# Kernel optimization log

Hardware: AMD Instinct MI355X
Metric: run time of the kernel (lower is better)

The kernel has to match this reference:

```python
import jax, jax.numpy as jnp
import numpy as np

NUM_GRAPHS = 8
NEG_SLOPE = 0.2  # PyG GATConv default negative_slope


def gat_dense(x, W, att_src, att_dst, W_edge, att_edge, bias, agg, mask):
    """Dense-masked equivalent of PyG GATConv(edge_dim=1, add_self_loops=True,
    fill_value='mean'). mask[i,j]=True means edge src=i -> dst=j."""
    N = x.shape[0]
    H, C = att_src.shape
    h = (x @ W).reshape(N, H, C)                      # [N,H,C]
    a_s = jnp.einsum('nhc,hc->nh', h, att_src)        # alpha_src per node
    a_d = jnp.einsum('nhc,hc->nh', h, att_dst)        # alpha_dst per node
    eye = jnp.eye(N, dtype=bool)
    mask_od = mask & ~eye                             # remove_self_loops
    ev = jnp.where(mask_od, agg, 0.0)                 # edge_attr (scalar per edge)
    cnt = mask_od.sum(axis=0)                         # in-degree per dst
    mean_e = jnp.where(cnt > 0, ev.sum(axis=0) / jnp.maximum(cnt, 1), 0.0)
    ev = ev + jnp.eye(N, dtype=agg.dtype) * mean_e    # add self-loops, fill='mean' per dst
    full = mask_od | eye
    # lin_edge is Linear(1, H*C, bias=False): per-head edge score is
    # e_ij * sum_c W_edge[h,c]*att_edge[h,c]
    we = (W_edge.reshape(H, C) * att_edge).sum(-1)    # [H]
    logits = jax.nn.leaky_relu(a_s[:, None, :] + a_d[None, :, :] + ev[:, :, None] * we[None, None, :], NEG_SLOPE)  # [src,dst,H]
    logits = jnp.where(full[:, :, None], logits, -jnp.inf)
    alpha = jax.nn.softmax(logits, axis=0)            # segment softmax over sources per dst
    out = jnp.einsum('sdh,shc->dhc', alpha, h).reshape(N, H * C) + bias
    return out


def setup_inputs() -> dict:
    key = jax.random.key(0)
    ks = jax.random.split(key, 20)
    N, IN, HID, H, OUT = 2048, 128, 64, 4, 10
    s = 0.05
    rn = lambda k, shp, sc=s: (jax.random.normal(k, shp, dtype=jnp.float32) * sc)
    return {
        'x': jax.random.normal(ks[0], (N, IN), dtype=jnp.float32),
        'attn_tensor': jax.random.normal(ks[1], (12, N, N), dtype=jnp.float32),
        'batch_idx': jnp.sort(jax.random.randint(ks[2], (N,), 0, NUM_GRAPHS)),
        # Conv2d(12,1,1) -> 1x1 conv == weighted sum over the 12 maps
        'w_agg': rn(ks[3], (12,), 0.2),
        'b_agg': jnp.zeros((), dtype=jnp.float32),
        # GAT layer 1: in=128 -> heads=4, out=64, concat
        'W1': rn(ks[4], (IN, H * HID)),
        'att_src1': rn(ks[5], (H, HID)),
        'att_dst1': rn(ks[6], (H, HID)),
        'We1': rn(ks[7], (1, H * HID)),
        'att_e1': rn(ks[8], (H, HID)),
        'bias1': jnp.zeros((H * HID,), dtype=jnp.float32),
        # GAT layer 2: in=256 -> heads=1, out=64
        'W2': rn(ks[9], (H * HID, HID)),
        'att_src2': rn(ks[10], (1, HID)),
        'att_dst2': rn(ks[11], (1, HID)),
        'We2': rn(ks[12], (1, HID)),
        'att_e2': rn(ks[13], (1, HID)),
        'bias2': jnp.zeros((HID,), dtype=jnp.float32),
        # final Linear(hidden, out)
        'W_lin': rn(ks[14], (HID, OUT)),
        'b_lin': jnp.zeros((OUT,), dtype=jnp.float32),
    }


def reference(x, attn_tensor, batch_idx, w_agg, b_agg, W1, att_src1, att_dst1,
              We1, att_e1, bias1, W2, att_src2, att_dst2, We2, att_e2, bias2,
              W_lin, b_lin):
    # 1x1 conv over the 12 attention maps -> [N,N]
    agg = jnp.einsum('k,kij->ij', w_agg, attn_tensor) + b_agg
    mask = agg > 0.0  # threshold
    h1 = jax.nn.elu(gat_dense(x, W1, att_src1, att_dst1, We1, att_e1, bias1, agg, mask))
    h2 = jax.nn.elu(gat_dense(h1, W2, att_src2, att_dst2, We2, att_e2, bias2, agg, mask))
    # global mean pool over graphs
    ones = jnp.ones((x.shape[0],), dtype=h2.dtype)
    cnt = jax.ops.segment_sum(ones, batch_idx, num_segments=NUM_GRAPHS)
    g = jax.ops.segment_sum(h2, batch_idx, num_segments=NUM_GRAPHS) / jnp.maximum(cnt, 1.0)[:, None]
    out = g @ W_lin + b_lin
    # edge_attr = agg[mask]; returned densely (masked) to keep static shapes
    edge_attr = jnp.where(mask, agg, 0.0)
    return out, edge_attr
```

## Files before the change

kernel.cpp:

```cpp
#include <hip/hip_runtime.h>

#define N 2048
#define NG 8

__device__ __forceinline__ float lrelu(float x) { return x > 0.f ? x : 0.2f * x; }

__global__ __launch_bounds__(256) void aggh1K(const float* __restrict__ attn,
                                              const float* __restrict__ w_agg,
                                              const float* __restrict__ b_agg,
                                              const float* __restrict__ x,
                                              const float* __restrict__ W1,
                                              const float* __restrict__ att_src1,
                                              const float* __restrict__ att_dst1,
                                              const float* __restrict__ We1, const float* __restrict__ att_e1,
                                              const float* __restrict__ We2, const float* __restrict__ att_e2,
                                              float* __restrict__ edge_out,
                                              float* __restrict__ colSum, float* __restrict__ colCnt,
                                              float* __restrict__ h1, float* __restrict__ a_s1, float* __restrict__ a_d1,
                                              float* __restrict__ we) {
  __shared__ float smem[512];
  int tid = threadIdx.x;
  if (blockIdx.x < 512) {
    float* xr = smem;
    int n0 = blockIdx.x * 4;
    if (blockIdx.x == 0) {
      float v1 = We1[tid] * att_e1[tid];
#pragma unroll
      for (int off = 32; off > 0; off >>= 1) v1 += __shfl_down(v1, off);
      int lane = tid & 63, wid = tid >> 6;
      if (lane == 0) we[wid] = v1;
      float v2 = (tid < 64) ? We2[tid] * att_e2[tid] : 0.f;
#pragma unroll
      for (int off = 32; off > 0; off >>= 1) v2 += __shfl_down(v2, off);
      if (tid == 0) we[4] = v2;
    }
    for (int t = tid; t < 512; t += 256) xr[t] = x[n0 * 128 + t];
    __syncthreads();
    float acc[4] = {0.f, 0.f, 0.f, 0.f};
    for (int k = 0; k < 128; ++k) {
      float wv = W1[k * 256 + tid];
#pragma unroll
      for (int r = 0; r < 4; ++r) acc[r] += xr[r * 128 + k] * wv;
    }
    float asw = att_src1[tid], adw = att_dst1[tid];
    int lane = tid & 63, head = tid >> 6;
#pragma unroll
    for (int r = 0; r < 4; ++r) {
      h1[(size_t)(n0 + r) * 256 + tid] = acc[r];
      float ps = acc[r] * asw, pd = acc[r] * adw;
#pragma unroll
      for (int off = 32; off > 0; off >>= 1) { ps += __shfl_down(ps, off); pd += __shfl_down(pd, off); }
      if (lane == 0) { a_s1[(n0 + r) * 4 + head] = ps; a_d1[(n0 + r) * 4 + head] = pd; }
    }
  } else {
    float* wsh = smem;
    float* cs = smem + 32;
    float* cc = smem + 64;
    int bidA = blockIdx.x - 512;
    int tx = tid & 31, ty = tid >> 5;
    if (tid < 12) wsh[tid] = w_agg[tid];
    if (tid < 32) { cs[tid] = 0.f; cc[tid] = 0.f; }
    __syncthreads();
    int i0 = (bidA >> 6) * 32, j0 = (bidA & 63) * 32;
    int j = j0 + tx;
    float bb = b_agg[0];
#pragma unroll
    for (int r = 0; r < 4; ++r) {
      int i = i0 + ty + 8 * r;
      const float* p = attn + (size_t)i * N + j;
      float v = bb;
#pragma unroll
      for (int k = 0; k < 12; ++k) v += wsh[k] * p[(size_t)k * N * N];
      float e = v > 0.f ? v : 0.f;
      edge_out[(size_t)i * N + j] = e;
      if (e > 0.f && i != j) { atomicAdd(&cs[tx], e); atomicAdd(&cc[tx], 1.f); }
    }
    __syncthreads();
    if (tid < 32) {
      atomicAdd(&colSum[j0 + tid], cs[tid]);
      atomicAdd(&colCnt[j0 + tid], cc[tid]);
    }
  }
}

__global__ __launch_bounds__(256) void pv1K(const float* __restrict__ edge, const float* __restrict__ h1,
                                            const float* __restrict__ a_s1, const float* __restrict__ a_d1,
                                            const float* __restrict__ colSum, const float* __restrict__ colCnt,
                                            const float* __restrict__ we,
                                            float* __restrict__ partials, float* __restrict__ z1) {
  __shared__ float hT[16][260];
  __shared__ float pL[16][260];
  int tid = threadIdx.x;
  int d0 = blockIdx.x * 64;
  int sBeg = blockIdx.y * 128;
  float w0 = we[0], w1 = we[1], w2 = we[2], w3 = we[3];
  int ssp = tid & 15, dq = tid >> 4;
  float4 ad4[4];
  float me_[4];
#pragma unroll
  for (int q = 0; q < 4; ++q) {
    int d = d0 + dq * 4 + q;
    ad4[q] = *(const float4*)(a_d1 + d * 4);
    float c = colCnt[d];
    me_[q] = c > 0.f ? colSum[d] / c : 0.f;
  }
  float zac[4][4];
#pragma unroll
  for (int q = 0; q < 4; ++q)
#pragma unroll
    for (int h = 0; h < 4; ++h) zac[q][h] = 0.f;
  int dg = tid & 7;
  int cb = (tid >> 3) * 8;
  int hh = tid >> 6;
  float acc[8][8];
#pragma unroll
  for (int i = 0; i < 8; ++i)
#pragma unroll
    for (int j = 0; j < 8; ++j) acc[i][j] = 0.f;

  int c4 = (tid & 63) * 4;
  int rb = (tid >> 6) * 4;

#pragma unroll 1
  for (int s0 = sBeg; s0 < sBeg + 128; s0 += 16) {
#pragma unroll
    for (int p4 = 0; p4 < 4; ++p4) {
      int r = rb + p4;
      *(float4*)(&hT[r][c4]) = *(const float4*)(h1 + (size_t)(s0 + r) * 256 + c4);
    }
    {
      int s = s0 + ssp;
      float4 as4 = *(const float4*)(a_s1 + s * 4);
      float4 av4 = *(const float4*)(edge + (size_t)s * N + d0 + dq * 4);
      float ev_[4] = {av4.x, av4.y, av4.z, av4.w};
      float pq[4][4];
#pragma unroll
      for (int q = 0; q < 4; ++q) {
        int d = d0 + dq * 4 + q;
        float av = ev_[q];
        float ev; bool inc;
        if (s == d) { ev = me_[q]; inc = true; } else { ev = av; inc = av > 0.f; }
        float p0 = inc ? __expf(lrelu(as4.x + ad4[q].x + ev * w0)) : 0.f;
        float p1 = inc ? __expf(lrelu(as4.y + ad4[q].y + ev * w1)) : 0.f;
        float p2 = inc ? __expf(lrelu(as4.z + ad4[q].z + ev * w2)) : 0.f;
        float p3 = inc ? __expf(lrelu(as4.w + ad4[q].w + ev * w3)) : 0.f;
        pq[0][q] = p0; pq[1][q] = p1; pq[2][q] = p2; pq[3][q] = p3;
        zac[q][0] += p0; zac[q][1] += p1; zac[q][2] += p2; zac[q][3] += p3;
      }
#pragma unroll
      for (int h = 0; h < 4; ++h)
        *(float4*)(&pL[ssp][h * 64 + dq * 4]) = make_float4(pq[h][0], pq[h][1], pq[h][2], pq[h][3]);
    }
    __syncthreads();
#pragma unroll
    for (int ss = 0; ss < 16; ++ss) {
      float4 pA = *(const float4*)(&pL[ss][hh * 64 + dg * 8]);
      float4 pB = *(const float4*)(&pL[ss][hh * 64 + dg * 8 + 4]);
      float4 hA = *(const float4*)(&hT[ss][cb]);
      float4 hB = *(const float4*)(&hT[ss][cb + 4]);
      float pv[8] = {pA.x, pA.y, pA.z, pA.w, pB.x, pB.y, pB.z, pB.w};
      float hv[8] = {hA.x, hA.y, hA.z, hA.w, hB.x, hB.y, hB.z, hB.w};
#pragma unroll
      for (int di = 0; di < 8; ++di)
#pragma unroll
        for (int ci = 0; ci < 8; ++ci) acc[di][ci] += pv[di] * hv[ci];
    }
    __syncthreads();
  }
  float* outp = partials + (size_t)blockIdx.y * ((size_t)N * 256);
#pragma unroll
  for (int di = 0; di < 8; ++di) {
    size_t rowo = (size_t)(d0 + dg * 8 + di) * 256 + cb;
    *(float4*)(outp + rowo) = make_float4(acc[di][0], acc[di][1], acc[di][2], acc[di][3]);
    *(float4*)(outp + rowo + 4) = make_float4(acc[di][4], acc[di][5], acc[di][6], acc[di][7]);
  }
#pragma unroll
  for (int q = 0; q < 4; ++q)
#pragma unroll
    for (int h = 0; h < 4; ++h) {
      float v = zac[q][h];
      v += __shfl_down(v, 8); v += __shfl_down(v, 4);
      v += __shfl_down(v, 2); v += __shfl_down(v, 1);
      if (ssp == 0) atomicAdd(&z1[(d0 + dq * 4 + q) * 4 + h], v);
    }
}

__global__ __launch_bounds__(256) void h2K(const float* __restrict__ partials, const float* __restrict__ z1,
                                           const float* __restrict__ bias1,
                                           const float* __restrict__ W2,
                                           const float* __restrict__ att_src2, const float* __restrict__ att_dst2,
                                           float* __restrict__ hh2, float* __restrict__ a_s2, float* __restrict__ a_d2) {
  __shared__ float hr[4][256];
  int tid = threadIdx.x;
  int n0 = blockIdx.x * 4;
  for (int e = tid; e < 1024; e += 256) {
    int node = e >> 8, c = e & 255;
    size_t base = (size_t)(n0 + node) * 256 + c;
    float sAcc = 0.f;
#pragma unroll
    for (int q = 0; q < 16; ++q) sAcc += partials[(size_t)q * N * 256 + base];
    float a = sAcc / z1[(n0 + node) * 4 + (c >> 6)] + bias1[c];
    hr[node][c] = a > 0.f ? a : __expf(a) - 1.f;
  }
  __syncthreads();
  int c = tid & 63, nl = tid >> 6;
  float acc = 0.f;
  for (int k = 0; k < 256; ++k) acc += hr[nl][k] * W2[k * 64 + c];
  hh2[(size_t)(n0 + nl) * 64 + c] = acc;
  float ps = acc * att_src2[c], pd = acc * att_dst2[c];
#pragma unroll
  for (int off = 32; off > 0; off >>= 1) { ps += __shfl_down(ps, off); pd += __shfl_down(pd, off); }
  if (c == 0) { a_s2[n0 + nl] = ps; a_d2[n0 + nl] = pd; }
}

__global__ __launch_bounds__(256) void pv2K(const float* __restrict__ edge, const float* __restrict__ hh2,
                                            const float* __restrict__ a_s2, const float* __restrict__ a_d2,
                                            const float* __restrict__ colSum, const float* __restrict__ colCnt,
                                            const float* __restrict__ we,
                                            float* __restrict__ partials, float* __restrict__ z2) {
  __shared__ float hT[16][68];
  __shared__ float pL[16][132];
  int tid = threadIdx.x;
  int d0 = blockIdx.x * 128;
  int sBeg = blockIdx.y * 64;
  float wE = we[4];
  int ssp = tid & 15, dq = tid >> 4;
  float adv[8], me_[8];
#pragma unroll
  for (int q = 0; q < 8; ++q) {
    int d = d0 + dq * 8 + q;
    adv[q] = a_d2[d];
    float c = colCnt[d];
    me_[q] = c > 0.f ? colSum[d] / c : 0.f;
  }
  float zac[8];
#pragma unroll
  for (int q = 0; q < 8; ++q) zac[q] = 0.f;
  int dg = tid & 15;
  int cg = tid >> 4;
  float acc[8][4];
#pragma unroll
  for (int i = 0; i < 8; ++i)
#pragma unroll
    for (int j = 0; j < 4; ++j) acc[i][j] = 0.f;

  int stR = tid >> 4, stC = (tid & 15) * 4;

#pragma unroll 1
  for (int s0 = sBeg; s0 < sBeg + 64; s0 += 16) {
    *(float4*)(&hT[stR][stC]) = *(const float4*)(hh2 + (size_t)(s0 + stR) * 64 + stC);
    {
      int s = s0 + ssp;
      float asv = a_s2[s];
      float4 eA = *(const float4*)(edge + (size_t)s * N + d0 + dq * 8);
      float4 eB = *(const float4*)(edge + (size_t)s * N + d0 + dq * 8 + 4);
      float ev_[8] = {eA.x, eA.y, eA.z, eA.w, eB.x, eB.y, eB.z, eB.w};
      float pq[8];
#pragma unroll
      for (int q = 0; q < 8; ++q) {
        int d = d0 + dq * 8 + q;
        float av = ev_[q];
        float ev; bool inc;
        if (s == d) { ev = me_[q]; inc = true; } else { ev = av; inc = av > 0.f; }
        float p = inc ? __expf(lrelu(asv + adv[q] + ev * wE)) : 0.f;
        pq[q] = p;
        zac[q] += p;
      }
      *(float4*)(&pL[ssp][dq * 8])     = make_float4(pq[0], pq[1], pq[2], pq[3]);
      *(float4*)(&pL[ssp][dq * 8 + 4]) = make_float4(pq[4], pq[5], pq[6], pq[7]);
    }
    __syncthreads();
#pragma unroll
    for (int ss = 0; ss < 16; ++ss) {
      float4 pA = *(const float4*)(&pL[ss][dg * 8]);
      float4 pB = *(const float4*)(&pL[ss][dg * 8 + 4]);
      float4 hA = *(const float4*)(&hT[ss][cg * 4]);
      float pv[8] = {pA.x, pA.y, pA.z, pA.w, pB.x, pB.y, pB.z, pB.w};
      float hv[4] = {hA.x, hA.y, hA.z, hA.w};
#pragma unroll
      for (int di = 0; di < 8; ++di)
#pragma unroll
        for (int ci = 0; ci < 4; ++ci) acc[di][ci] += pv[di] * hv[ci];
    }
    __syncthreads();
  }
  float* outp = partials + (size_t)blockIdx.y * ((size_t)N * 64);
#pragma unroll
  for (int di = 0; di < 8; ++di) {
    size_t rowo = (size_t)(d0 + dg * 8 + di) * 64 + cg * 4;
    *(float4*)(outp + rowo) = make_float4(acc[di][0], acc[di][1], acc[di][2], acc[di][3]);
  }
#pragma unroll
  for (int q = 0; q < 8; ++q) {
    float v = zac[q];
    v += __shfl_down(v, 8); v += __shfl_down(v, 4);
    v += __shfl_down(v, 2); v += __shfl_down(v, 1);
    if (ssp == 0) atomicAdd(&z2[d0 + dq * 8 + q], v);
  }
}

__global__ __launch_bounds__(256) void fin2poolK(const float* __restrict__ partials, const float* __restrict__ z2,
                                                 const float* __restrict__ bias2, const int* __restrict__ bidx,
                                                 const float* __restrict__ W_lin, const float* __restrict__ b_lin,
                                                 float* __restrict__ gsum, float* __restrict__ gcnt,
                                                 int* __restrict__ ticket, float* __restrict__ out) {
  int tid = threadIdx.x;
  int i = blockIdx.x * 256 + tid;
  int d = i >> 6, c = i & 63;
  float s = 0.f;
#pragma unroll
  for (int q = 0; q < 32; ++q) s += partials[(size_t)q * N * 64 + i];
  float a = s / z2[d] + bias2[c];
  float v = a > 0.f ? a : __expf(a) - 1.f;
  int g = bidx[d];
  atomicAdd(&gsum[g * 64 + c], v);
  if (c == 0) atomicAdd(&gcnt[g], 1.f);
  __threadfence();
  __syncthreads();
  __shared__ int lastSh;
  if (tid == 0) {
    int t = atomicAdd(ticket, 1);
    lastSh = (t == (int)gridDim.x - 1) ? 1 : 0;
  }
  __syncthreads();
  if (lastSh) {
    __shared__ float gm[NG][64];
    __shared__ float cnt_[NG];
    if (tid < NG) cnt_[tid] = atomicAdd(&gcnt[tid], 0.f);
    __syncthreads();
    for (int e = tid; e < NG * 64; e += 256) {
      float sv = atomicAdd(&gsum[e], 0.f);
      gm[e >> 6][e & 63] = sv / fmaxf(cnt_[e >> 6], 1.f);
    }
    __syncthreads();
    if (tid < NG * 10) {
      int b = tid / 10, o = tid % 10;
      float accv = b_lin[o];
      for (int k = 0; k < 64; ++k) accv += gm[b][k] * W_lin[k * 10 + o];
      out[b * 10 + o] = accv;
    }
  }
}

extern "C" void kernel_launch(void* const* d_in, const int* in_sizes, int n_in,
                              void* d_out, int out_size, void* d_ws, size_t ws_size,
                              hipStream_t stream) {
  const float* x        = (const float*)d_in[0];
  const float* attn     = (const float*)d_in[1];
  const int*   bidx     = (const int*)d_in[2];
  const float* w_agg    = (const float*)d_in[3];
  const float* b_agg    = (const float*)d_in[4];
  const float* W1       = (const float*)d_in[5];
  const float* att_src1 = (const float*)d_in[6];
  const float* att_dst1 = (const float*)d_in[7];
  const float* We1      = (const float*)d_in[8];
  const float* att_e1   = (const float*)d_in[9];
  const float* bias1    = (const float*)d_in[10];
  const float* W2       = (const float*)d_in[11];
  const float* att_src2 = (const float*)d_in[12];
  const float* att_dst2 = (const float*)d_in[13];
  const float* We2      = (const float*)d_in[14];
  const float* att_e2   = (const float*)d_in[15];
  const float* bias2    = (const float*)d_in[16];
  const float* W_lin    = (const float*)d_in[17];
  const float* b_lin    = (const float*)d_in[18];

  float* out = (float*)d_out;
  float* edge_out = out + 80;

  float* w = (float*)d_ws;
  size_t o = 0;
  float* zb   = w + o; o += 7 * N + 1024;
  float* wev  = w + o; o += 8;
  float* h1   = w + o; o += (size_t)N * 256;
  float* a_s1 = w + o; o += (size_t)N * 4;
  float* a_d1 = w + o; o += (size_t)N * 4;
  float* hh2  = w + o; o += (size_t)N * 64;
  float* a_s2 = w + o; o += N;
  float* a_d2 = w + o; o += N;
  float* partials = w + o; o += (size_t)16 * N * 256;

  float* colSum = zb;
  float* colCnt = zb + N;
  float* z1     = zb + 2 * N;
  float* z2     = zb + 6 * N;
  float* gsum   = zb + 7 * N;
  float* gcnt   = zb + 7 * N + 512;
  int*   ticket = (int*)(zb + 7 * N + 520);

  hipMemsetAsync(zb, 0, (7 * N + 1024) * sizeof(float), stream);
  aggh1K<<<4608, 256, 0, stream>>>(attn, w_agg, b_agg, x, W1, att_src1, att_dst1,
                                   We1, att_e1, We2, att_e2,
                                   edge_out, colSum, colCnt, h1, a_s1, a_d1, wev);
  pv1K<<<dim3(32, 16), 256, 0, stream>>>(edge_out, h1, a_s1, a_d1, colSum, colCnt, wev, partials, z1);
  h2K<<<512, 256, 0, stream>>>(partials, z1, bias1, W2, att_src2, att_dst2, hh2, a_s2, a_d2);
  pv2K<<<dim3(16, 32), 256, 0, stream>>>(edge_out, hh2, a_s2, a_d2, colSum, colCnt, wev, partials, z2);
  fin2poolK<<<512, 256, 0, stream>>>(partials, z2, bias2, bidx, W_lin, b_lin, gsum, gcnt, ticket, out);
}
```

Measured before the change: 481.6 us.

## Fuse all stages into one persistent kernel with software grid barriers

Replaces the memset plus five kernel launches with a single persistent kernel of 512 blocks that separates stages with an atomic-counter grid barrier. The edge aggregation is remapped so each block handles 32 rows by 256 columns, with column sums kept in registers. The pv1 stage stages h1 in two halves to fit shared memory at two blocks per CU. This is meant to remove launch overhead and inter-kernel gaps. In exchange the aggregation stage runs with far fewer blocks, the barriers add spin cost, and the design assumes all 512 blocks are co-resident.

```diff
diff --git a/kernel.cpp b/kernel.cpp
--- a/kernel.cpp
+++ b/kernel.cpp
@@ -2,342 +2,361 @@
 
 #define N 2048
 #define NG 8
+#define NBLK 512
 
 __device__ __forceinline__ float lrelu(float x) { return x > 0.f ? x : 0.2f * x; }
 
-__global__ __launch_bounds__(256) void aggh1K(const float* __restrict__ attn,
-                                              const float* __restrict__ w_agg,
-                                              const float* __restrict__ b_agg,
-                                              const float* __restrict__ x,
-                                              const float* __restrict__ W1,
-                                              const float* __restrict__ att_src1,
-                                              const float* __restrict__ att_dst1,
-                                              const float* __restrict__ We1, const float* __restrict__ att_e1,
-                                              const float* __restrict__ We2, const float* __restrict__ att_e2,
-                                              float* __restrict__ edge_out,
-                                              float* __restrict__ colSum, float* __restrict__ colCnt,
-                                              float* __restrict__ h1, float* __restrict__ a_s1, float* __restrict__ a_d1,
-                                              float* __restrict__ we) {
-  __shared__ float smem[512];
-  int tid = threadIdx.x;
-  if (blockIdx.x < 512) {
+__device__ int g_barCnt = 0;
+
+__device__ __forceinline__ void gridBarrier() {
+  __threadfence();
+  __syncthreads();
+  if (threadIdx.x == 0) {
+    int t = atomicAdd(&g_barCnt, 1) + 1;
+    int target = ((t - 1) / NBLK + 1) * NBLK;
+    if (t != target) {
+      while (atomicAdd(&g_barCnt, 0) < target) __builtin_amdgcn_s_sleep(16);
+    }
+  }
+  __syncthreads();
+  __threadfence();
+}
+
+struct KP {
+  const float* attn; const float* w_agg; const float* b_agg; const float* x;
+  const float* W1; const float* att_src1; const float* att_dst1;
+  const float* We1; const float* att_e1; const float* bias1;
+  const float* W2; const float* att_src2; const float* att_dst2;
+  const float* We2; const float* att_e2; const float* bias2;
+  const float* W_lin; const float* b_lin; const int* bidx;
+  float* edge_out; float* colSum; float* colCnt; float* z1; float* z2;
+  float* gsum; float* gcnt; float* wev;
+  float* h1; float* a_s1; float* a_d1; float* hh2; float* a_s2; float* a_d2;
+  float* partials; float* out;
+};
+
+__global__ __launch_bounds__(256, 2) void megaK(KP p) {
+  __shared__ float smem[6240];
+  const int tid = threadIdx.x;
+  const int b = blockIdx.x;
+
+  {
+    const int total = 7 * N + 520;
+    int i = b * 256 + tid;
+    if (i < total) p.colSum[i] = 0.f;
+  }
+  gridBarrier();
+
+  {
+    float wreg[12];
+#pragma unroll
+    for (int k = 0; k < 12; ++k) wreg[k] = p.w_agg[k];
+    const float bb = p.b_agg[0];
+    const int i0 = (b >> 3) * 32, j0 = (b & 7) * 256;
+    const int j = j0 + tid;
+    float csA = 0.f, ccA = 0.f;
+#pragma unroll 2
+    for (int r = 0; r < 32; ++r) {
+      int i = i0 + r;
+      const float* pp = p.attn + (size_t)i * N + j;
+      float v = bb;
+#pragma unroll
+      for (int k = 0; k < 12; ++k) v += wreg[k] * pp[(size_t)k * N * N];
+      float e = v > 0.f ? v : 0.f;
+      p.edge_out[(size_t)i * N + j] = e;
+      if (e > 0.f && i != j) { csA += e; ccA += 1.f; }
+    }
+    atomicAdd(&p.colSum[j], csA);
+    atomicAdd(&p.colCnt[j], ccA);
+
     float* xr = smem;
-    int n0 = blockIdx.x * 4;
-    if (blockIdx.x == 0) {
-      float v1 = We1[tid] * att_e1[tid];
+    const int n0 = b * 4;
+    if (b == 0) {
+      float v1 = p.We1[tid] * p.att_e1[tid];
 #pragma unroll
       for (int off = 32; off > 0; off >>= 1) v1 += __shfl_down(v1, off);
       int lane = tid & 63, wid = tid >> 6;
-      if (lane == 0) we[wid] = v1;
-      float v2 = (tid < 64) ? We2[tid] * att_e2[tid] : 0.f;
+      if (lane == 0) p.wev[wid] = v1;
+      float v2 = (tid < 64) ? p.We2[tid] * p.att_e2[tid] : 0.f;
 #pragma unroll
       for (int off = 32; off > 0; off >>= 1) v2 += __shfl_down(v2, off);
-      if (tid == 0) we[4] = v2;
-    }
-    for (int t = tid; t < 512; t += 256) xr[t] = x[n0 * 128 + t];
+      if (tid == 0) p.wev[4] = v2;
+    }
+    for (int t = tid; t < 512; t += 256) xr[t] = p.x[n0 * 128 + t];
     __syncthreads();
     float acc[4] = {0.f, 0.f, 0.f, 0.f};
     for (int k = 0; k < 128; ++k) {
-      float wv = W1[k * 256 + tid];
+      float wv = p.W1[k * 256 + tid];
 #pragma unroll
       for (int r = 0; r < 4; ++r) acc[r] += xr[r * 128 + k] * wv;
     }
-    float asw = att_src1[tid], adw = att_dst1[tid];
+    float asw = p.att_src1[tid], adw = p.att_dst1[tid];
     int lane = tid & 63, head = tid >> 6;
 #pragma unroll
     for (int r = 0; r < 4; ++r) {
-      h1[(size_t)(n0 + r) * 256 + tid] = acc[r];
+      p.h1[(size_t)(n0 + r) * 256 + tid] = acc[r];
       float ps = acc[r] * asw, pd = acc[r] * adw;
 #pragma unroll
       for (int off = 32; off > 0; off >>= 1) { ps += __shfl_down(ps, off); pd += __shfl_down(pd, off); }
-      if (lane == 0) { a_s1[(n0 + r) * 4 + head] = ps; a_d1[(n0 + r) * 4 + head] = pd; }
-    }
-  } else {
-    float* wsh = smem;
-    float* cs = smem + 32;
-    float* cc = smem + 64;
-    int bidA = blockIdx.x - 512;
-    int tx = tid & 31, ty = tid >> 5;
-    if (tid < 12) wsh[tid] = w_agg[tid];
-    if (tid < 32) { cs[tid] = 0.f; cc[tid] = 0.f; }
+      if (lane == 0) { p.a_s1[(n0 + r) * 4 + head] = ps; p.a_d1[(n0 + r) * 4 + head] = pd; }
+    }
+  }
+  gridBarrier();
+
+  {
+    const int bx = b & 31, by = b >> 5;
+    const int d0 = bx * 64;
+    const int sBeg = by * 128;
+    float (*hT)[260] = (float (*)[260])smem;
+    float (*pL)[260] = (float (*)[260])(smem + 2080);
+    float w0 = p.wev[0], w1 = p.wev[1], w2 = p.wev[2], w3 = p.wev[3];
+    int ssp = tid & 15, dq = tid >> 4;
+    float4 ad4[4];
+    float me_[4];
+#pragma unroll
+    for (int q = 0; q < 4; ++q) {
+      int d = d0 + dq * 4 + q;
+      ad4[q] = *(const float4*)(p.a_d1 + d * 4);
+      float c = p.colCnt[d];
+      me_[q] = c > 0.f ? p.colSum[d] / c : 0.f;
+    }
+    float zac[4][4];
+#pragma unroll
+    for (int q = 0; q < 4; ++q)
+#pragma unroll
+      for (int h = 0; h < 4; ++h) zac[q][h] = 0.f;
+    int dg = tid & 7;
+    int cb = (tid >> 3) * 8;
+    int hh = tid >> 6;
+    float acc[8][8];
+#pragma unroll
+    for (int i = 0; i < 8; ++i)
+#pragma unroll
+      for (int jj = 0; jj < 8; ++jj) acc[i][jj] = 0.f;
+
+    int c4 = (tid & 63) * 4;
+    int rb2 = (tid >> 6) * 2;
+
+#pragma unroll 1
+    for (int s0 = sBeg; s0 < sBeg + 128; s0 += 16) {
+      {
+        int s = s0 + ssp;
+        float4 as4 = *(const float4*)(p.a_s1 + s * 4);
+        float4 av4 = *(const float4*)(p.edge_out + (size_t)s * N + d0 + dq * 4);
+        float ev_[4] = {av4.x, av4.y, av4.z, av4.w};
+        float pq[4][4];
+#pragma unroll
+        for (int q = 0; q < 4; ++q) {
+          int d = d0 + dq * 4 + q;
+          float av = ev_[q];
+          float ev; bool inc;
+          if (s == d) { ev = me_[q]; inc = true; } else { ev = av; inc = av > 0.f; }
+          float p0 = inc ? __expf(lrelu(as4.x + ad4[q].x + ev * w0)) : 0.f;
+          float p1 = inc ? __expf(lrelu(as4.y + ad4[q].y + ev * w1)) : 0.f;
+          float p2 = inc ? __expf(lrelu(as4.z + ad4[q].z + ev * w2)) : 0.f;
+          float p3 = inc ? __expf(lrelu(as4.w + ad4[q].w + ev * w3)) : 0.f;
+          pq[0][q] = p0; pq[1][q] = p1; pq[2][q] = p2; pq[3][q] = p3;
+          zac[q][0] += p0; zac[q][1] += p1; zac[q][2] += p2; zac[q][3] += p3;
+        }
+#pragma unroll
+        for (int h = 0; h < 4; ++h)
+          *(float4*)(&pL[ssp][h * 64 + dq * 4]) = make_float4(pq[h][0], pq[h][1], pq[h][2], pq[h][3]);
+      }
+#pragma unroll
+      for (int p4 = 0; p4 < 2; ++p4) {
+        int r = rb2 + p4;
+        *(float4*)(&hT[r][c4]) = *(const float4*)(p.h1 + (size_t)(s0 + r) * 256 + c4);
+      }
+      __syncthreads();
+#pragma unroll
+      for (int ss = 0; ss < 8; ++ss) {
+        float4 pA = *(const float4*)(&pL[ss][hh * 64 + dg * 8]);
+        float4 pB = *(const float4*)(&pL[ss][hh * 64 + dg * 8 + 4]);
+        float4 hA = *(const float4*)(&hT[ss][cb]);
+        float4 hB = *(const float4*)(&hT[ss][cb + 4]);
+        float pv[8] = {pA.x, pA.y, pA.z, pA.w, pB.x, pB.y, pB.z, pB.w};
+        float hv[8] = {hA.x, hA.y, hA.z, hA.w, hB.x, hB.y, hB.z, hB.w};
+#pragma unroll
+        for (int di = 0; di < 8; ++di)
+#pragma unroll
+          for (int ci = 0; ci < 8; ++ci) acc[di][ci] += pv[di] * hv[ci];
+      }
+      __syncthreads();
+#pragma unroll
+      for (int p4 = 0; p4 < 2; ++p4) {
+        int r = rb2 + p4;
+        *(float4*)(&hT[r][c4]) = *(const float4*)(p.h1 + (size_t)(s0 + 8 + r) * 256 + c4);
+      }
+      __syncthreads();
+#pragma unroll
+      for (int ss = 8; ss < 16; ++ss) {
+        float4 pA = *(const float4*)(&pL[ss][hh * 64 + dg * 8]);
+        float4 pB = *(const float4*)(&pL[ss][hh * 64 + dg * 8 + 4]);
+        float4 hA = *(const float4*)(&hT[ss - 8][cb]);
+        float4 hB = *(const float4*)(&hT[ss - 8][cb + 4]);
+        float pv[8] = {pA.x, pA.y, pA.z, pA.w, pB.x, pB.y, pB.z, pB.w};
+        float hv[8] = {hA.x, hA.y, hA.z, hA.w, hB.x, hB.y, hB.z, hB.w};
+#pragma unroll
+        for (int di = 0; di < 8; ++di)
+#pragma unroll
+          for (int ci = 0; ci < 8; ++ci) acc[di][ci] += pv[di] * hv[ci];
+      }
+      __syncthreads();
+    }
+    float* outp = p.partials + (size_t)by * ((size_t)N * 256);
+#pragma unroll
+    for (int di = 0; di < 8; ++di) {
+      size_t rowo = (size_t)(d0 + dg * 8 + di) * 256 + cb;
+      *(float4*)(outp + rowo) = make_float4(acc[di][0], acc[di][1], acc[di][2], acc[di][3]);
+      *(float4*)(outp + rowo + 4) = make_float4(acc[di][4], acc[di][5], acc[di][6], acc[di][7]);
+    }
+#pragma unroll
+    for (int q = 0; q < 4; ++q)
+#pragma unroll
+      for (int h = 0; h < 4; ++h) {
+        float v = zac[q][h];
+        v += __shfl_down(v, 8); v += __shfl_down(v, 4);
+        v += __shfl_down(v, 2); v += __shfl_down(v, 1);
+        if (ssp == 0) atomicAdd(&p.z1[(d0 + dq * 4 + q) * 4 + h], v);
+      }
+  }
+  gridBarrier();
+
+  {
+    float (*hr)[256] = (float (*)[256])smem;
+    const int n0 = b * 4;
+    for (int e = tid; e < 1024; e += 256) {
+      int node = e >> 8, c = e & 255;
+      size_t base = (size_t)(n0 + node) * 256 + c;
+      float sAcc = 0.f;
+#pragma unroll
+      for (int q = 0; q < 16; ++q) sAcc += p.partials[(size_t)q * N * 256 + base];
+      float a = sAcc / p.z1[(n0 + node) * 4 + (c >> 6)] + p.bias1[c];
+      hr[node][c] = a > 0.f ? a : __expf(a) - 1.f;
+    }
     __syncthreads();
-    int i0 = (bidA >> 6) * 32, j0 = (bidA & 63) * 32;
-    int j = j0 + tx;
-    float bb = b_agg[0];
-#pragma unroll
-    for (int r = 0; r < 4; ++r) {
-      int i = i0 + ty + 8 * r;
-      const float* p = attn + (size_t)i * N + j;
-      float v = bb;
-#pragma unroll
-      for (int k = 0; k < 12; ++k) v += wsh[k] * p[(size_t)k * N * N];
-      float e = v > 0.f ? v : 0.f;
-      edge_out[(size_t)i * N + j] = e;
-      if (e > 0.f && i != j) { atomicAdd(&cs[tx], e); atomicAdd(&cc[tx], 1.f); }
-    }
-    __syncthreads();
-    if (tid < 32) {
-      atomicAdd(&colSum[j0 + tid], cs[tid]);
-      atomicAdd(&colCnt[j0 + tid], cc[tid]);
-    }
-  }
-}
-
-__global__ __launch_bounds__(256) void pv1K(const float* __restrict__ edge, const float* __restrict__ h1,
-                                            const float* __restrict__ a_s1, const float* __restrict__ a_d1,
-                                            const float* __restrict__ colSum, const float* __restrict__ colCnt,
-                                            const float* __restrict__ we,
-                                            float* __restrict__ partials, float* __restrict__ z1) {
-  __shared__ float hT[16][260];
-  __shared__ float pL[16][260];
-  int tid = threadIdx.x;
-  int d0 = blockIdx.x * 64;
-  int sBeg = blockIdx.y * 128;
-  float w0 = we[0], w1 = we[1], w2 = we[2], w3 = we[3];
-  int ssp = tid & 15, dq = tid >> 4;
-  float4 ad4[4];
-  float me_[4];
-#pragma unroll
-  for (int q = 0; q < 4; ++q) {
-    int d = d0 + dq * 4 + q;
-    ad4[q] = *(const float4*)(a_d1 + d * 4);
-    float c = colCnt[d];
-    me_[q] = c > 0.f ? colSum[d] / c : 0.f;
-  }
-  float zac[4][4];
-#pragma unroll
-  for (int q = 0; q < 4; ++q)
-#pragma unroll
-    for (int h = 0; h < 4; ++h) zac[q][h] = 0.f;
-  int dg = tid & 7;
-  int cb = (tid >> 3) * 8;
-  int hh = tid >> 6;
-  float acc[8][8];
-#pragma unroll
-  for (int i = 0; i < 8; ++i)
-#pragma unroll
-    for (int j = 0; j < 8; ++j) acc[i][j] = 0.f;
-
-  int c4 = (tid & 63) * 4;
-  int rb = (tid >> 6) * 4;
+    int c = tid & 63, nl = tid >> 6;
+    float acc = 0.f;
+    for (int k = 0; k < 256; ++k) acc += hr[nl][k] * p.W2[k * 64 + c];
+    p.hh2[(size_t)(n0 + nl) * 64 + c] = acc;
+    float ps = acc * p.att_src2[c], pd = acc * p.att_dst2[c];
+#pragma unroll
+    for (int off = 32; off > 0; off >>= 1) { ps += __shfl_down(ps, off); pd += __shfl_down(pd, off); }
+    if (c == 0) { p.a_s2[n0 + nl] = ps; p.a_d2[n0 + nl] = pd; }
+  }
+  gridBarrier();
+
+  {
+    const int bx = b & 15, by = b >> 4;
+    const int d0 = bx * 128;
+    const int sBeg = by * 64;
+    float (*hT)[68]  = (float (*)[68])smem;
+    float (*pL)[132] = (float (*)[132])(smem + 1088);
+    float wE = p.wev[4];
+    int ssp = tid & 15, dq = tid >> 4;
+    float adv[8], me_[8];
+#pragma unroll
+    for (int q = 0; q < 8; ++q) {
+      int d = d0 + dq * 8 + q;
+      adv[q] = p.a_d2[d];
+      float c = p.colCnt[d];
+      me_[q] = c > 0.f ? p.colSum[d] / c : 0.f;
+    }
+    float zac[8];
+#pragma unroll
+    for (int q = 0; q < 8; ++q) zac[q] = 0.f;
+    int dg = tid & 15;
+    int cg2 = tid >> 4;
+    float acc[8][4];
+#pragma unroll
+    for (int i = 0; i < 8; ++i)
+#pragma unroll
+      for (int jj = 0; jj < 4; ++jj) acc[i][jj] = 0.f;
+
+    int stR = tid >> 4, stC = (tid & 15) * 4;
 
 #pragma unroll 1
-  for (int s0 = sBeg; s0 < sBeg + 128; s0 += 16) {
-#pragma unroll
-    for (int p4 = 0; p4 < 4; ++p4) {
-      int r = rb + p4;
-      *(float4*)(&hT[r][c4]) = *(const float4*)(h1 + (size_t)(s0 + r) * 256 + c4);
-    }
-    {
-      int s = s0 + ssp;
-      float4 as4 = *(const float4*)(a_s1 + s * 4);
-      float4 av4 = *(const float4*)(edge + (size_t)s * N + d0 + dq * 4);
-      float ev_[4] = {av4.x, av4.y, av4.z, av4.w};
-      float pq[4][4];
-#pragma unroll
-      for (int q = 0; q < 4; ++q) {
-        int d = d0 + dq * 4 + q;
-        float av = ev_[q];
-        float ev; bool inc;
-        if (s == d) { ev = me_[q]; inc = true; } else { ev = av; inc = av > 0.f; }
-        float p0 = inc ? __expf(lrelu(as4.x + ad4[q].x + ev * w0)) : 0.f;
-        float p1 = inc ? __expf(lrelu(as4.y + ad4[q].y + ev * w1)) : 0.f;
-        float p2 = inc ? __expf(lrelu(as4.z + ad4[q].z + ev * w2)) : 0.f;
-        float p3 = inc ? __expf(lrelu(as4.w + ad4[q].w + ev * w3)) : 0.f;
-        pq[0][q] = p0; pq[1][q] = p1; pq[2][q] = p2; pq[3][q] = p3;
-        zac[q][0] += p0; zac[q][1] += p1; zac[q][2] += p2; zac[q][3] += p3;
-      }
-#pragma unroll
-      for (int h = 0; h < 4; ++h)
-        *(float4*)(&pL[ssp][h * 64 + dq * 4]) = make_float4(pq[h][0], pq[h][1], pq[h][2], pq[h][3]);
-    }
-    __syncthreads();
-#pragma unroll
-    for (int ss = 0; ss < 16; ++ss) {
-      float4 pA = *(const float4*)(&pL[ss][hh * 64 + dg * 8]);
-      float4 pB = *(const float4*)(&pL[ss][hh * 64 + dg * 8 + 4]);
-      float4 hA = *(const float4*)(&hT[ss][cb]);
-      float4 hB = *(const float4*)(&hT[ss][cb + 4]);
-      float pv[8] = {pA.x, pA.y, pA.z, pA.w, pB.x, pB.y, pB.z, pB.w};
-      float hv[8] = {hA.x, hA.y, hA.z, hA.w, hB.x, hB.y, hB.z, hB.w};
-#pragma unroll
-      for (int di = 0; di < 8; ++di)
-#pragma unroll
-        for (int ci = 0; ci < 8; ++ci) acc[di][ci] += pv[di] * hv[ci];
-    }
-    __syncthreads();
-  }
-  float* outp = partials + (size_t)blockIdx.y * ((size_t)N * 256);
-#pragma unroll
-  for (int di = 0; di < 8; ++di) {
-    size_t rowo = (size_t)(d0 + dg * 8 + di) * 256 + cb;
-    *(float4*)(outp + rowo) = make_float4(acc[di][0], acc[di][1], acc[di][2], acc[di][3]);
-    *(float4*)(outp + rowo + 4) = make_float4(acc[di][4], acc[di][5], acc[di][6], acc[di][7]);
-  }
-#pragma unroll
-  for (int q = 0; q < 4; ++q)
-#pragma unroll
-    for (int h = 0; h < 4; ++h) {
-      float v = zac[q][h];
+    for (int s0 = sBeg; s0 < sBeg + 64; s0 += 16) {
+      *(float4*)(&hT[stR][stC]) = *(const float4*)(p.hh2 + (size_t)(s0 + stR) * 64 + stC);
+      {
+        int s = s0 + ssp;
+        float asv = p.a_s2[s];
+        float4 eA = *(const float4*)(p.edge_out + (size_t)s * N + d0 + dq * 8);
+        float4 eB = *(const float4*)(p.edge_out + (size_t)s * N + d0 + dq * 8 + 4);
+        float ev_[8] = {eA.x, eA.y, eA.z, eA.w, eB.x, eB.y, eB.z, eB.w};
+        float pq[8];
+#pragma unroll
+        for (int q = 0; q < 8; ++q) {
+          int d = d0 + dq * 8 + q;
+          float av = ev_[q];
+          float ev; bool inc;
+          if (s == d) { ev = me_[q]; inc = true; } else { ev = av; inc = av > 0.f; }
+          float pz = inc ? __expf(lrelu(asv + adv[q] + ev * wE)) : 0.f;
+          pq[q] = pz;
+          zac[q] += pz;
+        }
+        *(float4*)(&pL[ssp][dq * 8])     = make_float4(pq[0], pq[1], pq[2], pq[3]);
+        *(float4*)(&pL[ssp][dq * 8 + 4]) = make_float4(pq[4], pq[5], pq[6], pq[7]);
+      }
+      __syncthreads();
+#pragma unroll
+      for (int ss = 0; ss < 16; ++ss) {
+        float4 pA = *(const float4*)(&pL[ss][dg * 8]);
+        float4 pB = *(const float4*)(&pL[ss][dg * 8 + 4]);
+        float4 hA = *(const float4*)(&hT[ss][cg2 * 4]);
+        float pv[8] = {pA.x, pA.y, pA.z, pA.w, pB.x, pB.y, pB.z, pB.w};
+        float hv[4] = {hA.x, hA.y, hA.z, hA.w};
+#pragma unroll
+        for (int di = 0; di < 8; ++di)
+#pragma unroll
+          for (int ci = 0; ci < 4; ++ci) acc[di][ci] += pv[di] * hv[ci];
+      }
+      __syncthreads();
+    }
+    float* outp = p.partials + (size_t)by * ((size_t)N * 64);
+#pragma unroll
+    for (int di = 0; di < 8; ++di) {
+      size_t rowo = (size_t)(d0 + dg * 8 + di) * 64 + cg2 * 4;
+      *(float4*)(outp + rowo) = make_float4(acc[di][0], acc[di][1], acc[di][2], acc[di][3]);
+    }
+#pragma unroll
+    for (int q = 0; q < 8; ++q) {
+      float v = zac[q];
       v += __shfl_down(v, 8); v += __shfl_down(v, 4);
       v += __shfl_down(v, 2); v += __shfl_down(v, 1);
-      if (ssp == 0) atomicAdd(&z1[(d0 + dq * 4 + q) * 4 + h], v);
-    }
-}
-
-__global__ __launch_bounds__(256) void h2K(const float* __restrict__ partials, const float* __restrict__ z1,
-                                           const float* __restrict__ bias1,
-                                           const float* __restrict__ W2,
-                                           const float* __restrict__ att_src2, const float* __restrict__ att_dst2,
-                                           float* __restrict__ hh2, float* __restrict__ a_s2, float* __restrict__ a_d2) {
-  __shared__ float hr[4][256];
-  int tid = threadIdx.x;
-  int n0 = blockIdx.x * 4;
-  for (int e = tid; e < 1024; e += 256) {
-    int node = e >> 8, c = e & 255;
-    size_t base = (size_t)(n0 + node) * 256 + c;
-    float sAcc = 0.f;
-#pragma unroll
-    for (int q = 0; q < 16; ++q) sAcc += partials[(size_t)q * N * 256 + base];
-    float a = sAcc / z1[(n0 + node) * 4 + (c >> 6)] + bias1[c];
-    hr[node][c] = a > 0.f ? a : __expf(a) - 1.f;
-  }
-  __syncthreads();
-  int c = tid & 63, nl = tid >> 6;
-  float acc = 0.f;
-  for (int k = 0; k < 256; ++k) acc += hr[nl][k] * W2[k * 64 + c];
-  hh2[(size_t)(n0 + nl) * 64 + c] = acc;
-  float ps = acc * att_src2[c], pd = acc * att_dst2[c];
-#pragma unroll
-  for (int off = 32; off > 0; off >>= 1) { ps += __shfl_down(ps, off); pd += __shfl_down(pd, off); }
-  if (c == 0) { a_s2[n0 + nl] = ps; a_d2[n0 + nl] = pd; }
-}
-
-__global__ __launch_bounds__(256) void pv2K(const float* __restrict__ edge, const float* __restrict__ hh2,
-                                            const float* __restrict__ a_s2, const float* __restrict__ a_d2,
-                                            const float* __restrict__ colSum, const float* __restrict__ colCnt,
-                                            const float* __restrict__ we,
-                                            float* __restrict__ partials, float* __restrict__ z2) {
-  __shared__ float hT[16][68];
-  __shared__ float pL[16][132];
-  int tid = threadIdx.x;
-  int d0 = blockIdx.x * 128;
-  int sBeg = blockIdx.y * 64;
-  float wE = we[4];
-  int ssp = tid & 15, dq = tid >> 4;
-  float adv[8], me_[8];
-#pragma unroll
-  for (int q = 0; q < 8; ++q) {
-    int d = d0 + dq * 8 + q;
-    adv[q] = a_d2[d];
-    float c = colCnt[d];
-    me_[q] = c > 0.f ? colSum[d] / c : 0.f;
-  }
-  float zac[8];
-#pragma unroll
-  for (int q = 0; q < 8; ++q) zac[q] = 0.f;
-  int dg = tid & 15;
-  int cg = tid >> 4;
-  float acc[8][4];
-#pragma unroll
-  for (int i = 0; i < 8; ++i)
-#pragma unroll
-    for (int j = 0; j < 4; ++j) acc[i][j] = 0.f;
-
-  int stR = tid >> 4, stC = (tid & 15) * 4;
-
-#pragma unroll 1
-  for (int s0 = sBeg; s0 < sBeg + 64; s0 += 16) {
-    *(float4*)(&hT[stR][stC]) = *(const float4*)(hh2 + (size_t)(s0 + stR) * 64 + stC);
-    {
-      int s = s0 + ssp;
-      float asv = a_s2[s];
-      float4 eA = *(const float4*)(edge + (size_t)s * N + d0 + dq * 8);
-      float4 eB = *(const float4*)(edge + (size_t)s * N + d0 + dq * 8 + 4);
-      float ev_[8] = {eA.x, eA.y, eA.z, eA.w, eB.x, eB.y, eB.z, eB.w};
-      float pq[8];
-#pragma unroll
-      for (int q = 0; q < 8; ++q) {
-        int d = d0 + dq * 8 + q;
-        float av = ev_[q];
-        float ev; bool inc;
-        if (s == d) { ev = me_[q]; inc = true; } else { ev = av; inc = av > 0.f; }
-        float p = inc ? __expf(lrelu(asv + adv[q] + ev * wE)) : 0.f;
-        pq[q] = p;
-        zac[q] += p;
-      }
-      *(float4*)(&pL[ssp][dq * 8])     = make_float4(pq[0], pq[1], pq[2], pq[3]);
-      *(float4*)(&pL[ssp][dq * 8 + 4]) = make_float4(pq[4], pq[5], pq[6], pq[7]);
-    }
-    __syncthreads();
-#pragma unroll
-    for (int ss = 0; ss < 16; ++ss) {
-      float4 pA = *(const float4*)(&pL[ss][dg * 8]);
-      float4 pB = *(const float4*)(&pL[ss][dg * 8 + 4]);
-      float4 hA = *(const float4*)(&hT[ss][cg * 4]);
-      float pv[8] = {pA.x, pA.y, pA.z, pA.w, pB.x, pB.y, pB.z, pB.w};
-      float hv[4] = {hA.x, hA.y, hA.z, hA.w};
-#pragma unroll
-      for (int di = 0; di < 8; ++di)
-#pragma unroll
-        for (int ci = 0; ci < 4; ++ci) acc[di][ci] += pv[di] * hv[ci];
-    }
-    __syncthreads();
-  }
-  float* outp = partials + (size_t)blockIdx.y * ((size_t)N * 64);
-#pragma unroll
-  for (int di = 0; di < 8; ++di) {
-    size_t rowo = (size_t)(d0 + dg * 8 + di) * 64 + cg * 4;
-    *(float4*)(outp + rowo) = make_float4(acc[di][0], acc[di][1], acc[di][2], acc[di][3]);
-  }
-#pragma unroll
-  for (int q = 0; q < 8; ++q) {
-    float v = zac[q];
-    v += __shfl_down(v, 8); v += __shfl_down(v, 4);
-    v += __shfl_down(v, 2); v += __shfl_down(v, 1);
-    if (ssp == 0) atomicAdd(&z2[d0 + dq * 8 + q], v);
-  }
-}
-
-__global__ __launch_bounds__(256) void fin2poolK(const float* __restrict__ partials, const float* __restrict__ z2,
-                                                 const float* __restrict__ bias2, const int* __restrict__ bidx,
-                                                 const float* __restrict__ W_lin, const float* __restrict__ b_lin,
-                                                 float* __restrict__ gsum, float* __restrict__ gcnt,
-                                                 int* __restrict__ ticket, float* __restrict__ out) {
-  int tid = threadIdx.x;
-  int i = blockIdx.x * 256 + tid;
-  int d = i >> 6, c = i & 63;
-  float s = 0.f;
-#pragma unroll
-  for (int q = 0; q < 32; ++q) s += partials[(size_t)q * N * 64 + i];
-  float a = s / z2[d] + bias2[c];
-  float v = a > 0.f ? a : __expf(a) - 1.f;
-  int g = bidx[d];
-  atomicAdd(&gsum[g * 64 + c], v);
-  if (c == 0) atomicAdd(&gcnt[g], 1.f);
-  __threadfence();
-  __syncthreads();
-  __shared__ int lastSh;
-  if (tid == 0) {
-    int t = atomicAdd(ticket, 1);
-    lastSh = (t == (int)gridDim.x - 1) ? 1 : 0;
-  }
-  __syncthreads();
-  if (lastSh) {
-    __shared__ float gm[NG][64];
-    __shared__ float cnt_[NG];
-    if (tid < NG) cnt_[tid] = atomicAdd(&gcnt[tid], 0.f);
+      if (ssp == 0) atomicAdd(&p.z2[d0 + dq * 8 + q], v);
+    }
+  }
+  gridBarrier();
+
+  {
+    int i = b * 256 + tid;
+    int d = i >> 6, c = i & 63;
+    float s = 0.f;
+#pragma unroll
+    for (int q = 0; q < 32; ++q) s += p.partials[(size_t)q * N * 64 + i];
+    float a = s / p.z2[d] + p.bias2[c];
+    float v = a > 0.f ? a : __expf(a) - 1.f;
+    int g = p.bidx[d];
+    atomicAdd(&p.gsum[g * 64 + c], v);
+    if (c == 0) atomicAdd(&p.gcnt[g], 1.f);
+  }
+  gridBarrier();
+
+  if (b == 0) {
+    float* gm   = smem;
+    float* cnt_ = smem + 512;
+    if (tid < NG) cnt_[tid] = p.gcnt[tid];
     __syncthreads();
     for (int e = tid; e < NG * 64; e += 256) {
-      float sv = atomicAdd(&gsum[e], 0.f);
-      gm[e >> 6][e & 63] = sv / fmaxf(cnt_[e >> 6], 1.f);
+      gm[e] = p.gsum[e] / fmaxf(cnt_[e >> 6], 1.f);
     }
     __syncthreads();
     if (tid < NG * 10) {
-      int b = tid / 10, o = tid % 10;
-      float accv = b_lin[o];
-      for (int k = 0; k < 64; ++k) accv += gm[b][k] * W_lin[k * 10 + o];
-      out[b * 10 + o] = accv;
+      int bb2 = tid / 10, oo = tid % 10;
+      float accv = p.b_lin[oo];
+      for (int k = 0; k < 64; ++k) accv += gm[bb2 * 64 + k] * p.W_lin[k * 10 + oo];
+      p.out[bb2 * 10 + oo] = accv;
     }
   }
 }
@@ -345,55 +364,49 @@
 extern "C" void kernel_launch(void* const* d_in, const int* in_sizes, int n_in,
                               void* d_out, int out_size, void* d_ws, size_t ws_size,
                               hipStream_t stream) {
-  const float* x        = (const float*)d_in[0];
-  const float* attn     = (const float*)d_in[1];
-  const int*   bidx     = (const int*)d_in[2];
-  const float* w_agg    = (const float*)d_in[3];
-  const float* b_agg    = (const float*)d_in[4];
-  const float* W1       = (const float*)d_in[5];
-  const float* att_src1 = (const float*)d_in[6];
-  const float* att_dst1 = (const float*)d_in[7];
-  const float* We1      = (const float*)d_in[8];
-  const float* att_e1   = (const float*)d_in[9];
-  const float* bias1    = (const float*)d_in[10];
-  const float* W2       = (const float*)d_in[11];
-  const float* att_src2 = (const float*)d_in[12];
-  const float* att_dst2 = (const float*)d_in[13];
-  const float* We2      = (const float*)d_in[14];
-  const float* att_e2   = (const float*)d_in[15];
-  const float* bias2    = (const float*)d_in[16];
-  const float* W_lin    = (const float*)d_in[17];
-  const float* b_lin    = (const float*)d_in[18];
+  KP hp;
+  hp.x        = (const float*)d_in[0];
+  hp.attn     = (const float*)d_in[1];
+  hp.bidx     = (const int*)d_in[2];
+  hp.w_agg    = (const float*)d_in[3];
+  hp.b_agg    = (const float*)d_in[4];
+  hp.W1       = (const float*)d_in[5];
+  hp.att_src1 = (const float*)d_in[6];
+  hp.att_dst1 = (const float*)d_in[7];
+  hp.We1      = (const float*)d_in[8];
+  hp.att_e1   = (const float*)d_in[9];
+  hp.bias1    = (const float*)d_in[10];
+  hp.W2       = (const float*)d_in[11];
+  hp.att_src2 = (const float*)d_in[12];
+  hp.att_dst2 = (const float*)d_in[13];
+  hp.We2      = (const float*)d_in[14];
+  hp.att_e2   = (const float*)d_in[15];
+  hp.bias2    = (const float*)d_in[16];
+  hp.W_lin    = (const float*)d_in[17];
+  hp.b_lin    = (const float*)d_in[18];
 
   float* out = (float*)d_out;
-  float* edge_out = out + 80;
+  hp.out = out;
+  hp.edge_out = out + 80;
 
   float* w = (float*)d_ws;
   size_t o = 0;
-  float* zb   = w + o; o += 7 * N + 1024;
-  float* wev  = w + o; o += 8;
-  float* h1   = w + o; o += (size_t)N * 256;
-  float* a_s1 = w + o; o += (size_t)N * 4;
-  float* a_d1 = w + o; o += (size_t)N * 4;
-  float* hh2  = w + o; o += (size_t)N * 64;
-  float* a_s2 = w + o; o += N;
-  float* a_d2 = w + o; o += N;
-  float* partials = w + o; o += (size_t)16 * N * 256;
-
-  float* colSum = zb;
-  float* colCnt = zb + N;
-  float* z1     = zb + 2 * N;
-  float* z2     = zb + 6 * N;
-  float* gsum   = zb + 7 * N;
-  float* gcnt   = zb + 7 * N + 512;
-  int*   ticket = (int*)(zb + 7 * N + 520);
-
-  hipMemsetAsync(zb, 0, (7 * N + 1024) * sizeof(float), stream);
-  aggh1K<<<4608, 256, 0, stream>>>(attn, w_agg, b_agg, x, W1, att_src1, att_dst1,
-                                   We1, att_e1, We2, att_e2,
-                                   edge_out, colSum, colCnt, h1, a_s1, a_d1, wev);
-  pv1K<<<dim3(32, 16), 256, 0, stream>>>(edge_out, h1, a_s1, a_d1, colSum, colCnt, wev, partials, z1);
-  h2K<<<512, 256, 0, stream>>>(partials, z1, bias1, W2, att_src2, att_dst2, hh2, a_s2, a_d2);
-  pv2K<<<dim3(16, 32), 256, 0, stream>>>(edge_out, hh2, a_s2, a_d2, colSum, colCnt, wev, partials, z2);
-  fin2poolK<<<512, 256, 0, stream>>>(partials, z2, bias2, bidx, W_lin, b_lin, gsum, gcnt, ticket, out);
+  float* zb = w + o; o += 7 * N + 1024;
+  hp.wev  = w + o; o += 8;
+  hp.h1   = w + o; o += (size_t)N * 256;
+  hp.a_s1 = w + o; o += (size_t)N * 4;
+  hp.a_d1 = w + o; o += (size_t)N * 4;
+  hp.hh2  = w + o; o += (size_t)N * 64;
+  hp.a_s2 = w + o; o += N;
+  hp.a_d2 = w + o; o += N;
+  hp.partials = w + o; o += (size_t)16 * N * 256;
+
+  hp.colSum = zb;
+  hp.colCnt = zb + N;
+  hp.z1     = zb + 2 * N;
+  hp.z2     = zb + 6 * N;
+  hp.gsum   = zb + 7 * N;
+  hp.gcnt   = zb + 7 * N + 512;
+
+  megaK<<<dim3(NBLK), dim3(256), 0, stream>>>(hp);
 }
```

Measured after the change: 1.015 ms. 2.11x slower.
